# Kernel optimization log

Hardware: AMD Instinct MI355X
Metric: run time of the kernel (lower is better)

## Reference

```python
import jax, jax.numpy as jnp
import numpy as np

N_NODES = 100000
N_EDGES = 1600000
IN_CH, HID_CH, OUT_CH = 128, 256, 128


def _sage_conv(x, src, dst, W_l, b_l, W_r, n_nodes):
    """PyG SAGEConv with mean aggregation: lin_l(mean_j x_j) + lin_r(x)."""
    # gather source features per edge, scatter-sum into destination nodes
    agg = jax.ops.segment_sum(x[src], dst, num_segments=n_nodes)  # [N, C]
    deg = jax.ops.segment_sum(jnp.ones((src.shape[0],), x.dtype), dst,
                              num_segments=n_nodes)               # [N]
    mean = agg / jnp.maximum(deg, 1.0)[:, None]
    return mean @ W_l + b_l + x @ W_r


def setup_inputs() -> dict:
    key = jax.random.key(0)
    ks = jax.random.split(key, 8)
    x = jax.random.normal(ks[0], (N_NODES, IN_CH), dtype=jnp.float32)
    edge_index = jax.random.randint(ks[1], (2, N_EDGES), 0, N_NODES, dtype=jnp.int64)
    s1 = 1.0 / np.sqrt(IN_CH)
    s2 = 1.0 / np.sqrt(HID_CH)
    W1_l = jax.random.normal(ks[2], (IN_CH, HID_CH), dtype=jnp.float32) * s1
    W1_r = jax.random.normal(ks[3], (IN_CH, HID_CH), dtype=jnp.float32) * s1
    b1 = jnp.zeros((HID_CH,), dtype=jnp.float32)
    W2_l = jax.random.normal(ks[4], (HID_CH, OUT_CH), dtype=jnp.float32) * s2
    W2_r = jax.random.normal(ks[5], (HID_CH, OUT_CH), dtype=jnp.float32) * s2
    b2 = jnp.zeros((OUT_CH,), dtype=jnp.float32)
    return {"x": x, "edge_index": edge_index, "W1_l": W1_l, "b1": b1,
            "W1_r": W1_r, "W2_l": W2_l, "b2": b2, "W2_r": W2_r}


def reference(x, edge_index, W1_l, b1, W1_r, W2_l, b2, W2_r):
    src, dst = edge_index[0], edge_index[1]
    h = _sage_conv(x, src, dst, W1_l, b1, W1_r, N_NODES)
    h = jax.nn.relu(h)
    out = _sage_conv(h, src, dst, W2_l, b2, W2_r, N_NODES)
    return out
```

## Files before the change

kernel.cpp:

```cpp
#include <hip/hip_runtime.h>
#include <cstddef>

#define N_NODES_C 100000
#define N_EDGES_C 1600000

#define NPB 64
#define NB 1563
#define SENT_ROW 100000

#define NCB 392
#define CAP 5120
#define SC_EPB 4096
#define SC_BLOCKS 391

#define CONV1_BLOCKS 1563
#define CONV2_BLOCKS 1562

typedef unsigned short u16;
typedef __attribute__((ext_vector_type(8))) short bf16x8;
typedef __attribute__((ext_vector_type(4))) float f32x4;

__device__ __forceinline__ u16 f2bf(float f) {
    unsigned u = __float_as_uint(f);
    u += 0x7fffu + ((u >> 16) & 1);
    return (u16)(u >> 16);
}
__device__ __forceinline__ float lo16f(unsigned v) {
    return __uint_as_float(v << 16);
}
__device__ __forceinline__ float hi16f(unsigned v) {
    return __uint_as_float(v & 0xffff0000u);
}

__device__ __forceinline__ void conv_chunk(const float* __restrict__ x,
                                           u16* __restrict__ x_bf, int i) {
    float4 v = ((const float4*)x)[i];
    ushort4 o;
    o.x = f2bf(v.x); o.y = f2bf(v.y); o.z = f2bf(v.z); o.w = f2bf(v.w);
    ((ushort4*)x_bf)[i] = o;
}


__global__ __launch_bounds__(1024) void prep_a(
    const float* __restrict__ W1l, const float* __restrict__ W1r,
    const float* __restrict__ W2l, const float* __restrict__ W2r,
    u16* __restrict__ T1l, u16* __restrict__ T1r,
    u16* __restrict__ T2l, u16* __restrict__ T2r,
    int* __restrict__ ccursor, u16* __restrict__ x_bf, u16* __restrict__ p2z) {
    const int b = blockIdx.x;
    const int t = threadIdx.x;
    if (b < 128) {
        int id = b * 1024 + t;
        int which = id >> 15;
        int r = id & 32767;
        if (which == 0) {
            int n = r >> 7, k = r & 127;
            T1l[r] = f2bf(W1l[k * 256 + n]);
        } else if (which == 1) {
            int n = r >> 7, k = r & 127;
            T1r[r] = f2bf(W1r[k * 256 + n]);
        } else if (which == 2) {
            int n = r >> 8, k = r & 255;
            T2l[r] = f2bf(W2l[k * 128 + n]);
        } else {
            int n = r >> 8, k = r & 255;
            T2r[r] = f2bf(W2r[k * 128 + n]);
        }
    } else {
        if (t < NCB) ccursor[t] = 0;
        uint4 z; z.x = 0; z.y = 0; z.z = 0; z.w = 0;
        if (t >= 512 && t < 528)
            ((uint4*)(x_bf + (size_t)SENT_ROW * 128))[t - 512] = z;
        else if (t >= 528 && t < 544)
            ((uint4*)(p2z + (size_t)SENT_ROW * 128))[t - 528] = z;
    }
}


__global__ __launch_bounds__(1024) void scatter_conv(
    const int* __restrict__ src, const int* __restrict__ dst,
    int* __restrict__ ccursor, unsigned* __restrict__ epkt2,
    const float* __restrict__ x, u16* __restrict__ x_bf) {
    __shared__ unsigned spkt[SC_EPB];
    __shared__ unsigned short scb[SC_EPB];
    __shared__ int hist[NCB], lstart[NCB], lcur[NCB], grun[NCB], stmp[NCB];

    const int t = threadIdx.x;
    const int b = blockIdx.x;
    if (b >= SC_BLOCKS) {
        conv_chunk(x, x_bf, (b - SC_BLOCKS) * 1024 + t);
        return;
    }
    const int e0 = b * SC_EPB;
    const int cnt = min(SC_EPB, N_EDGES_C - e0);

    if (t < NCB) hist[t] = 0;
    __syncthreads();

    int4 dd, ss;
    int i4 = (e0 >> 2) + t;
    int vi = (i4 * 4 < N_EDGES_C);
    if (vi) {
        dd = ((const int4*)dst)[i4];
        ss = ((const int4*)src)[i4];
        atomicAdd(&hist[dd.x >> 8], 1);
        atomicAdd(&hist[dd.y >> 8], 1);
        atomicAdd(&hist[dd.z >> 8], 1);
        atomicAdd(&hist[dd.w >> 8], 1);
    }
    __syncthreads();

    if (t < NCB) stmp[t] = hist[t];
    __syncthreads();
    for (int off = 1; off < NCB; off <<= 1) {
        int v = 0;
        if (t < NCB && t >= off) v = stmp[t - off];
        __syncthreads();
        if (t < NCB) stmp[t] += v;
        __syncthreads();
    }
    if (t < NCB) {
        int excl = stmp[t] - hist[t];
        lstart[t] = excl;
        lcur[t] = excl;
        if (hist[t])
            grun[t] = t * CAP + atomicAdd(&ccursor[t], hist[t]);
    }
    __syncthreads();

    if (vi) {
        {
            int cb = dd.x >> 8;
            int pos = atomicAdd(&lcur[cb], 1);
            spkt[pos] = ((unsigned)(dd.x & 255) << 17) | (unsigned)ss.x;
            scb[pos] = (unsigned short)cb;
        }
        {
            int cb = dd.y >> 8;
            int pos = atomicAdd(&lcur[cb], 1);
            spkt[pos] = ((unsigned)(dd.y & 255) << 17) | (unsigned)ss.y;
            scb[pos] = (unsigned short)cb;
        }
        {
            int cb = dd.z >> 8;
            int pos = atomicAdd(&lcur[cb], 1);
            spkt[pos] = ((unsigned)(dd.z & 255) << 17) | (unsigned)ss.z;
            scb[pos] = (unsigned short)cb;
        }
        {
            int cb = dd.w >> 8;
            int pos = atomicAdd(&lcur[cb], 1);
            spkt[pos] = ((unsigned)(dd.w & 255) << 17) | (unsigned)ss.w;
            scb[pos] = (unsigned short)cb;
        }
    }
    __syncthreads();

#pragma unroll
    for (int k = 0; k < SC_EPB / 1024; ++k) {
        int i = k * 1024 + t;
        if (i < cnt) {
            int cb = scb[i];
            epkt2[grun[cb] + (i - lstart[cb])] = spkt[i];
        }
    }
}


__global__ __launch_bounds__(1024) void sort_conv(
    const int* __restrict__ ccursor, const unsigned* __restrict__ epkt2,
    unsigned* __restrict__ esrc, int* __restrict__ deg, int* __restrict__ base,
    const float* __restrict__ x, u16* __restrict__ x_bf) {
    __shared__ int hist[256], lstart[256], lcur[256], stmp[256];
    const int t = threadIdx.x;
    const int c = blockIdx.x;
    if (c >= NCB) {
        conv_chunk(x, x_bf, 1600512 + (c - NCB) * 1024 + t);
        return;
    }
    const int s0 = c * CAP;
    int cnt = ccursor[c];
    if (cnt > CAP) cnt = CAP;

    if (t < 256) hist[t] = 0;
    __syncthreads();

    for (int i = t; i < cnt; i += 1024)
        atomicAdd(&hist[epkt2[s0 + i] >> 17], 1);
    __syncthreads();

    if (t < 256) stmp[t] = hist[t];
    __syncthreads();
    for (int off = 1; off < 256; off <<= 1) {
        int v = 0;
        if (t < 256 && t >= off) v = stmp[t - off];
        __syncthreads();
        if (t < 256) stmp[t] += v;
        __syncthreads();
    }
    if (t < 256) {
        int excl = stmp[t] - hist[t];
        lstart[t] = excl;
        lcur[t] = excl;
        int node = c * 256 + t;
        if (node < N_NODES_C) {
            deg[node] = hist[t];
            base[node] = s0 + excl;
        }
    }
    __syncthreads();

    for (int i = t; i < cnt; i += 1024) {
        unsigned p = epkt2[s0 + i];
        int pos = atomicAdd(&lcur[p >> 17], 1);
        esrc[s0 + pos] = p & 0x1ffffu;
    }
}


__global__ __launch_bounds__(512, 8) void fused_gemm_agg(
    const u16* __restrict__ x_bf, const int* __restrict__ deg,
    const int* __restrict__ base, const unsigned* __restrict__ esrc,
    const u16* __restrict__ T1l, const u16* __restrict__ T1r,
    const u16* __restrict__ T2l, const u16* __restrict__ T2r,
    const float* __restrict__ b1, const float* __restrict__ b2,
    u16* __restrict__ p2, u16* __restrict__ outp, int M) {
    alignas(16) __shared__ u16 uni[64 * 256];
    alignas(16) __shared__ u16 Bs[4096];

    u16* const meanS = uni;
    u16* const xS = uni + 64 * 128;
    u16* const hfrag = uni;

    const int tid = threadIdx.x;
    const int lane = tid & 63;
    const int wave = tid >> 6;
    const int qm = lane & 15;
    const int quad = lane >> 4;
    const int b = blockIdx.x;
    const int m0 = b * 64;

#pragma unroll
    for (int r = 0; r < 2; ++r) {
        int c = r * 512 + tid;
        int row = c >> 4, q16 = c & 15;
        __builtin_amdgcn_global_load_lds(
            (const __attribute__((address_space(1))) unsigned*)(
                x_bf + (size_t)(m0 + row) * 128 + ((q16 ^ (row & 7)) * 8)),
            (__attribute__((address_space(3))) unsigned*)(xS + c * 8), 16, 0, 0);
    }

    const int li8 = qm * 8;
    const int gbase = lane & 48;

    for (int pass = 0; pass < 2; ++pass) {
        int n = pass * 32 + wave * 4 + quad;
        int node = m0 + n;
        int d = 0, s0 = 0;
        if (node < N_NODES_C) { d = deg[node]; s0 = base[node]; }
        int dmax = max(d, __shfl_xor(d, 16, 64));
        dmax = max(dmax, __shfl_xor(dmax, 32, 64));

        float a0 = 0.f, a1 = 0.f, a2 = 0.f, a3 = 0.f;
        float a4 = 0.f, a5 = 0.f, a6 = 0.f, a7 = 0.f;

        for (int j = 0; j < dmax; j += 16) {
            int jj = j + qm;
            unsigned sidx = (jj < d) ? esrc[s0 + jj] : (unsigned)SENT_ROW;
            for (int u = 0; u < 16 && j + u < dmax; u += 4) {
                unsigned i0 = __shfl(sidx, gbase + u, 64);
                unsigned i1 = __shfl(sidx, gbase + u + 1, 64);
                unsigned i2 = __shfl(sidx, gbase + u + 2, 64);
                unsigned i3 = __shfl(sidx, gbase + u + 3, 64);
                uint4 r0 = *(const uint4*)(x_bf + (size_t)i0 * 128 + li8);
                uint4 r1 = *(const uint4*)(x_bf + (size_t)i1 * 128 + li8);
                uint4 r2 = *(const uint4*)(x_bf + (size_t)i2 * 128 + li8);
                uint4 r3 = *(const uint4*)(x_bf + (size_t)i3 * 128 + li8);
                a0 += lo16f(r0.x); a1 += hi16f(r0.x);
                a2 += lo16f(r0.y); a3 += hi16f(r0.y);
                a4 += lo16f(r0.z); a5 += hi16f(r0.z);
                a6 += lo16f(r0.w); a7 += hi16f(r0.w);
                a0 += lo16f(r1.x); a1 += hi16f(r1.x);
                a2 += lo16f(r1.y); a3 += hi16f(r1.y);
                a4 += lo16f(r1.z); a5 += hi16f(r1.z);
                a6 += lo16f(r1.w); a7 += hi16f(r1.w);
                a0 += lo16f(r2.x); a1 += hi16f(r2.x);
                a2 += lo16f(r2.y); a3 += hi16f(r2.y);
                a4 += lo16f(r2.z); a5 += hi16f(r2.z);
                a6 += lo16f(r2.w); a7 += hi16f(r2.w);
                a0 += lo16f(r3.x); a1 += hi16f(r3.x);
                a2 += lo16f(r3.y); a3 += hi16f(r3.y);
                a4 += lo16f(r3.z); a5 += hi16f(r3.z);
                a6 += lo16f(r3.w); a7 += hi16f(r3.w);
            }
        }

        float inv = d > 0 ? 1.f / (float)d : 0.f;
        uint4 o;
        o.x = (unsigned)f2bf(a0 * inv) | ((unsigned)f2bf(a1 * inv) << 16);
        o.y = (unsigned)f2bf(a2 * inv) | ((unsigned)f2bf(a3 * inv) << 16);
        o.z = (unsigned)f2bf(a4 * inv) | ((unsigned)f2bf(a5 * inv) << 16);
        o.w = (unsigned)f2bf(a6 * inv) | ((unsigned)f2bf(a7 * inv) << 16);
        *(uint4*)(meanS + n * 128 + ((qm ^ (n & 7)) * 8)) = o;
    }
    __syncthreads();

    const int wr0 = (wave >> 1) * 16;
    const int wcA = (wave & 1) * 64;
    f32x4 acch[8];
#pragma unroll
    for (int j = 0; j < 8; ++j) acch[j] = (f32x4){0.f, 0.f, 0.f, 0.f};

#pragma unroll
    for (int mat = 0; mat < 2; ++mat) {
        const u16* __restrict__ W = mat ? T1r : T1l;
        const u16* Al = mat ? xS : meanS;
#pragma unroll
        for (int k0 = 0; k0 < 128; k0 += 32) {
            int ch0 = k0 >> 3;
            int rowA = wr0 + qm;
            bf16x8 af = *(const bf16x8*)(Al + rowA * 128 +
                                         (((ch0 + quad) ^ (rowA & 7)) * 8));
#pragma unroll
            for (int h = 0; h < 2; ++h) {
                {
                    int c = tid;
                    int row = c >> 2, kc = c & 3;
                    __builtin_amdgcn_global_load_lds(
                        (const __attribute__((address_space(1))) unsigned*)(
                            W + (size_t)(h * 128 + row) * 128 + k0 +
                            ((kc ^ (row & 3)) * 8)),
                        (__attribute__((address_space(3))) unsigned*)(Bs + c * 8),
                        16, 0, 0);
                }
                __syncthreads();
#pragma unroll
                for (int j = 0; j < 4; ++j) {
                    int rB = wcA + j * 16 + qm;
                    bf16x8 bv = *(const bf16x8*)(Bs + rB * 32 +
                                                 ((quad ^ (rB & 3)) * 8));
                    acch[h * 4 + j] = __builtin_amdgcn_mfma_f32_16x16x32_bf16(
                        af, bv, acch[h * 4 + j], 0, 0, 0);
                }
                __syncthreads();
            }
        }
    }

#pragma unroll
    for (int h = 0; h < 2; ++h) {
#pragma unroll
        for (int j = 0; j < 4; ++j) {
            int n = h * 128 + wcA + j * 16 + qm;
            float bb = b1[n];
            int ks = n >> 5, quadB = (n >> 3) & 3, jB = n & 7;
#pragma unroll
            for (int r = 0; r < 4; ++r) {
                int mloc = wr0 + quad * 4 + r;
                float v = fmaxf(acch[h * 4 + j][r] + bb, 0.f);
                hfrag[((ks * 4 + (mloc >> 4)) * 16 + (mloc & 15)) * 32 +
                      quadB * 8 + jB] = f2bf(v);
            }
        }
    }
    __syncthreads();

    const int wrB = (wave >> 1) * 16;
    const int wcB = (wave & 1) * 64;
    f32x4 accp[4], acco[4];
#pragma unroll
    for (int j = 0; j < 4; ++j) {
        accp[j] = (f32x4){0.f, 0.f, 0.f, 0.f};
        acco[j] = (f32x4){0.f, 0.f, 0.f, 0.f};
    }

#pragma unroll
    for (int ks = 0; ks < 8; ++ks) {
        bf16x8 af = *(const bf16x8*)(hfrag +
                                     ((ks * 4 + (wrB >> 4)) * 16 + qm) * 32 + quad * 8);
#pragma unroll
        for (int half = 0; half < 2; ++half) {
            const u16* W = half ? T2r : T2l;
            {
                int c = tid;
                int row = c >> 2, kc = c & 3;
                __builtin_amdgcn_global_load_lds(
                    (const __attribute__((address_space(1))) unsigned*)(
                        W + (size_t)row * 256 + ks * 32 + ((kc ^ (row & 3)) * 8)),
                    (__attribute__((address_space(3))) unsigned*)(Bs + c * 8),
                    16, 0, 0);
            }
            __syncthreads();
            f32x4* acc = half ? acco : accp;
#pragma unroll
            for (int j = 0; j < 4; ++j) {
                int rB = wcB + j * 16 + qm;
                bf16x8 bv = *(const bf16x8*)(Bs + rB * 32 +
                                             ((quad ^ (rB & 3)) * 8));
                acc[j] = __builtin_amdgcn_mfma_f32_16x16x32_bf16(af, bv,
                                                                 acc[j], 0, 0, 0);
            }
            __syncthreads();
        }
    }

#pragma unroll
    for (int j = 0; j < 4; ++j) {
        int n = wcB + j * 16 + qm;
        float bb2 = b2[n];
#pragma unroll
        for (int r = 0; r < 4; ++r) {
            int row = m0 + wrB + quad * 4 + r;
            if (row < M) {
                p2[(size_t)row * 128 + n] = f2bf(accp[j][r]);
                outp[(size_t)row * 128 + n] = f2bf(acco[j][r] + bb2);
            }
        }
    }
}


__global__ __launch_bounds__(256, 8) void agg_final(const u16* __restrict__ tbl,
                                                    const int* __restrict__ deg,
                                                    const int* __restrict__ base,
                                                    const unsigned* __restrict__ esrc,
                                                    const u16* __restrict__ resid,
                                                    float* __restrict__ outv) {
    const int t = threadIdx.x;
    const int wave = t >> 6;
    const int lane = t & 63;
    const int qm = lane & 15;
    const int quad = lane >> 4;
    const int b = blockIdx.x;
    const int li8 = qm * 8;
    const int gbase = lane & 48;

    for (int pass = 0; pass < 4; ++pass) {
        int n = pass * 16 + wave * 4 + quad;
        int node = b * NPB + n;
        bool valid = node < N_NODES_C;
        int d = 0, s0 = 0;
        if (valid) { d = deg[node]; s0 = base[node]; }
        int dmax = max(d, __shfl_xor(d, 16, 64));
        dmax = max(dmax, __shfl_xor(dmax, 32, 64));

        float a0 = 0.f, a1 = 0.f, a2 = 0.f, a3 = 0.f;
        float a4 = 0.f, a5 = 0.f, a6 = 0.f, a7 = 0.f;

        for (int j = 0; j < dmax; j += 16) {
            int jj = j + qm;
            unsigned sidx = (jj < d) ? esrc[s0 + jj] : (unsigned)SENT_ROW;
            for (int u = 0; u < 16 && j + u < dmax; u += 4) {
                unsigned i0 = __shfl(sidx, gbase + u, 64);
                unsigned i1 = __shfl(sidx, gbase + u + 1, 64);
                unsigned i2 = __shfl(sidx, gbase + u + 2, 64);
                unsigned i3 = __shfl(sidx, gbase + u + 3, 64);
                uint4 r0 = *(const uint4*)(tbl + (size_t)i0 * 128 + li8);
                uint4 r1 = *(const uint4*)(tbl + (size_t)i1 * 128 + li8);
                uint4 r2 = *(const uint4*)(tbl + (size_t)i2 * 128 + li8);
                uint4 r3 = *(const uint4*)(tbl + (size_t)i3 * 128 + li8);
                a0 += lo16f(r0.x); a1 += hi16f(r0.x);
                a2 += lo16f(r0.y); a3 += hi16f(r0.y);
                a4 += lo16f(r0.z); a5 += hi16f(r0.z);
                a6 += lo16f(r0.w); a7 += hi16f(r0.w);
                a0 += lo16f(r1.x); a1 += hi16f(r1.x);
                a2 += lo16f(r1.y); a3 += hi16f(r1.y);
                a4 += lo16f(r1.z); a5 += hi16f(r1.z);
                a6 += lo16f(r1.w); a7 += hi16f(r1.w);
                a0 += lo16f(r2.x); a1 += hi16f(r2.x);
                a2 += lo16f(r2.y); a3 += hi16f(r2.y);
                a4 += lo16f(r2.z); a5 += hi16f(r2.z);
                a6 += lo16f(r2.w); a7 += hi16f(r2.w);
                a0 += lo16f(r3.x); a1 += hi16f(r3.x);
                a2 += lo16f(r3.y); a3 += hi16f(r3.y);
                a4 += lo16f(r3.z); a5 += hi16f(r3.z);
                a6 += lo16f(r3.w); a7 += hi16f(r3.w);
            }
        }

        if (valid) {
            float inv = d > 0 ? 1.f / (float)d : 0.f;
            uint4 rp = *(const uint4*)(resid + (size_t)node * 128 + li8);
            float* op = outv + (size_t)node * 128 + li8;
            float4 o0, o1;
            o0.x = a0 * inv + lo16f(rp.x);
            o0.y = a1 * inv + hi16f(rp.x);
            o0.z = a2 * inv + lo16f(rp.y);
            o0.w = a3 * inv + hi16f(rp.y);
            o1.x = a4 * inv + lo16f(rp.z);
            o1.y = a5 * inv + hi16f(rp.z);
            o1.z = a6 * inv + lo16f(rp.w);
            o1.w = a7 * inv + hi16f(rp.w);
            *(float4*)op = o0;
            *(float4*)(op + 4) = o1;
        }
    }
}


extern "C" void kernel_launch(void* const* d_in, const int* in_sizes, int n_in,
                              void* d_out, int out_size, void* d_ws, size_t ws_size,
                              hipStream_t stream) {
    const float* x = (const float*)d_in[0];
    const int* ei = (const int*)d_in[1];
    const float* W1l = (const float*)d_in[2];
    const float* b1 = (const float*)d_in[3];
    const float* W1r = (const float*)d_in[4];
    const float* W2l = (const float*)d_in[5];
    const float* b2 = (const float*)d_in[6];
    const float* W2r = (const float*)d_in[7];
    float* out = (float*)d_out;

    const int* src = ei;
    const int* dst = ei + N_EDGES_C;

    int* iw = (int*)d_ws;
    int* ccursor = iw;
    int* deg = iw + 512;
    int* base = iw + 100864;
    unsigned* epkt2 = (unsigned*)(iw + 201216);
    unsigned* esrc = (unsigned*)(iw + 2208256);
    u16* T1l = (u16*)(iw + 4215296);
    u16* T1r = T1l + 32768;
    u16* T2l = T1r + 32768;
    u16* T2r = T2l + 32768;
    u16* ub = (u16*)((char*)d_ws + (20u << 20));
    u16* x_bf = ub;
    u16* p2 = ub + 12850000;
    u16* outp = ub + 25700000;

    prep_a<<<129, 1024, 0, stream>>>(W1l, W1r, W2l, W2r, T1l, T1r, T2l, T2r,
                                     ccursor, x_bf, p2);
    scatter_conv<<<SC_BLOCKS + CONV1_BLOCKS, 1024, 0, stream>>>(
        src, dst, ccursor, epkt2, x, x_bf);
    sort_conv<<<NCB + CONV2_BLOCKS, 1024, 0, stream>>>(
        ccursor, epkt2, esrc, deg, base, x, x_bf);

    fused_gemm_agg<<<NB, 512, 0, stream>>>(x_bf, deg, base, esrc, T1l, T1r, T2l,
                                           T2r, b1, b2, p2, outp, N_NODES_C);
    agg_final<<<NB, 256, 0, stream>>>(p2, deg, base, esrc, outp, out);
}
```

Baseline: 331.0 us.

## Merge weight prep into scatter kernel and double edges per scatter block

Removes the separate prep_a launch: the weight transpose and bf16 conversion and the sentinel-row zeroing now run as extra blocks inside scatter_conv, and ccursor is cleared with hipMemsetAsync. Each scatter block now handles 8192 edges (two int4 loads per thread), which halves the scatter block count and the per-block histogram and scan overhead. The goal is fewer kernel launches and less fixed cost per block. It adds a memset node, doubles shared memory use per scatter block, and may lower occupancy.

```diff
diff --git a/kernel.cpp b/kernel.cpp
--- a/kernel.cpp
+++ b/kernel.cpp
@@ -10,9 +10,10 @@
 
 #define NCB 392
 #define CAP 5120
-#define SC_EPB 4096
-#define SC_BLOCKS 391
-
+#define SC_EPB 8192
+#define SC_BLOCKS 196
+
+#define WB_BLOCKS 128
 #define CONV1_BLOCKS 1563
 #define CONV2_BLOCKS 1562
 
@@ -41,46 +42,14 @@
 }
 
 
-__global__ __launch_bounds__(1024) void prep_a(
+__global__ __launch_bounds__(1024) void scatter_conv(
+    const int* __restrict__ src, const int* __restrict__ dst,
+    int* __restrict__ ccursor, unsigned* __restrict__ epkt2,
     const float* __restrict__ W1l, const float* __restrict__ W1r,
     const float* __restrict__ W2l, const float* __restrict__ W2r,
     u16* __restrict__ T1l, u16* __restrict__ T1r,
     u16* __restrict__ T2l, u16* __restrict__ T2r,
-    int* __restrict__ ccursor, u16* __restrict__ x_bf, u16* __restrict__ p2z) {
-    const int b = blockIdx.x;
-    const int t = threadIdx.x;
-    if (b < 128) {
-        int id = b * 1024 + t;
-        int which = id >> 15;
-        int r = id & 32767;
-        if (which == 0) {
-            int n = r >> 7, k = r & 127;
-            T1l[r] = f2bf(W1l[k * 256 + n]);
-        } else if (which == 1) {
-            int n = r >> 7, k = r & 127;
-            T1r[r] = f2bf(W1r[k * 256 + n]);
-        } else if (which == 2) {
-            int n = r >> 8, k = r & 255;
-            T2l[r] = f2bf(W2l[k * 128 + n]);
-        } else {
-            int n = r >> 8, k = r & 255;
-            T2r[r] = f2bf(W2r[k * 128 + n]);
-        }
-    } else {
-        if (t < NCB) ccursor[t] = 0;
-        uint4 z; z.x = 0; z.y = 0; z.z = 0; z.w = 0;
-        if (t >= 512 && t < 528)
-            ((uint4*)(x_bf + (size_t)SENT_ROW * 128))[t - 512] = z;
-        else if (t >= 528 && t < 544)
-            ((uint4*)(p2z + (size_t)SENT_ROW * 128))[t - 528] = z;
-    }
-}
-
-
-__global__ __launch_bounds__(1024) void scatter_conv(
-    const int* __restrict__ src, const int* __restrict__ dst,
-    int* __restrict__ ccursor, unsigned* __restrict__ epkt2,
-    const float* __restrict__ x, u16* __restrict__ x_bf) {
+    const float* __restrict__ x, u16* __restrict__ x_bf, u16* __restrict__ p2z) {
     __shared__ unsigned spkt[SC_EPB];
     __shared__ unsigned short scb[SC_EPB];
     __shared__ int hist[NCB], lstart[NCB], lcur[NCB], grun[NCB], stmp[NCB];
@@ -88,7 +57,32 @@
     const int t = threadIdx.x;
     const int b = blockIdx.x;
     if (b >= SC_BLOCKS) {
-        conv_chunk(x, x_bf, (b - SC_BLOCKS) * 1024 + t);
+        if (b < SC_BLOCKS + WB_BLOCKS) {
+            int id = (b - SC_BLOCKS) * 1024 + t;
+            int which = id >> 15;
+            int r = id & 32767;
+            if (which == 0) {
+                int n = r >> 7, k = r & 127;
+                T1l[r] = f2bf(W1l[k * 256 + n]);
+            } else if (which == 1) {
+                int n = r >> 7, k = r & 127;
+                T1r[r] = f2bf(W1r[k * 256 + n]);
+            } else if (which == 2) {
+                int n = r >> 8, k = r & 255;
+                T2l[r] = f2bf(W2l[k * 128 + n]);
+            } else {
+                int n = r >> 8, k = r & 255;
+                T2r[r] = f2bf(W2r[k * 128 + n]);
+            }
+        } else if (b == SC_BLOCKS + WB_BLOCKS) {
+            uint4 z; z.x = 0; z.y = 0; z.z = 0; z.w = 0;
+            if (t < 16)
+                ((uint4*)(x_bf + (size_t)SENT_ROW * 128))[t] = z;
+            else if (t < 32)
+                ((uint4*)(p2z + (size_t)SENT_ROW * 128))[t - 16] = z;
+        } else {
+            conv_chunk(x, x_bf, (b - SC_BLOCKS - WB_BLOCKS - 1) * 1024 + t);
+        }
         return;
     }
     const int e0 = b * SC_EPB;
@@ -97,16 +91,20 @@
     if (t < NCB) hist[t] = 0;
     __syncthreads();
 
-    int4 dd, ss;
-    int i4 = (e0 >> 2) + t;
-    int vi = (i4 * 4 < N_EDGES_C);
-    if (vi) {
-        dd = ((const int4*)dst)[i4];
-        ss = ((const int4*)src)[i4];
-        atomicAdd(&hist[dd.x >> 8], 1);
-        atomicAdd(&hist[dd.y >> 8], 1);
-        atomicAdd(&hist[dd.z >> 8], 1);
-        atomicAdd(&hist[dd.w >> 8], 1);
+    int4 dd[2], ss[2];
+    int vi[2];
+#pragma unroll
+    for (int r = 0; r < 2; ++r) {
+        int i = (e0 >> 2) + r * 1024 + t;
+        vi[r] = (i * 4 < N_EDGES_C);
+        if (vi[r]) {
+            dd[r] = ((const int4*)dst)[i];
+            ss[r] = ((const int4*)src)[i];
+            atomicAdd(&hist[dd[r].x >> 8], 1);
+            atomicAdd(&hist[dd[r].y >> 8], 1);
+            atomicAdd(&hist[dd[r].z >> 8], 1);
+            atomicAdd(&hist[dd[r].w >> 8], 1);
+        }
     }
     __syncthreads();
 
@@ -128,30 +126,35 @@
     }
     __syncthreads();
 
-    if (vi) {
-        {
-            int cb = dd.x >> 8;
-            int pos = atomicAdd(&lcur[cb], 1);
-            spkt[pos] = ((unsigned)(dd.x & 255) << 17) | (unsigned)ss.x;
-            scb[pos] = (unsigned short)cb;
-        }
-        {
-            int cb = dd.y >> 8;
-            int pos = atomicAdd(&lcur[cb], 1);
-            spkt[pos] = ((unsigned)(dd.y & 255) << 17) | (unsigned)ss.y;
-            scb[pos] = (unsigned short)cb;
-        }
-        {
-            int cb = dd.z >> 8;
-            int pos = atomicAdd(&lcur[cb], 1);
-            spkt[pos] = ((unsigned)(dd.z & 255) << 17) | (unsigned)ss.z;
-            scb[pos] = (unsigned short)cb;
-        }
-        {
-            int cb = dd.w >> 8;
-            int pos = atomicAdd(&lcur[cb], 1);
-            spkt[pos] = ((unsigned)(dd.w & 255) << 17) | (unsigned)ss.w;
-            scb[pos] = (unsigned short)cb;
+#pragma unroll
+    for (int r = 0; r < 2; ++r) {
+        if (vi[r]) {
+            int4 d = dd[r];
+            int4 s4 = ss[r];
+            {
+                int cb = d.x >> 8;
+                int pos = atomicAdd(&lcur[cb], 1);
+                spkt[pos] = ((unsigned)(d.x & 255) << 17) | (unsigned)s4.x;
+                scb[pos] = (unsigned short)cb;
+            }
+            {
+                int cb = d.y >> 8;
+                int pos = atomicAdd(&lcur[cb], 1);
+                spkt[pos] = ((unsigned)(d.y & 255) << 17) | (unsigned)s4.y;
+                scb[pos] = (unsigned short)cb;
+            }
+            {
+                int cb = d.z >> 8;
+                int pos = atomicAdd(&lcur[cb], 1);
+                spkt[pos] = ((unsigned)(d.z & 255) << 17) | (unsigned)s4.z;
+                scb[pos] = (unsigned short)cb;
+            }
+            {
+                int cb = d.w >> 8;
+                int pos = atomicAdd(&lcur[cb], 1);
+                spkt[pos] = ((unsigned)(d.w & 255) << 17) | (unsigned)s4.w;
+                scb[pos] = (unsigned short)cb;
+            }
         }
     }
     __syncthreads();
@@ -529,10 +532,11 @@
     u16* p2 = ub + 12850000;
     u16* outp = ub + 25700000;
 
-    prep_a<<<129, 1024, 0, stream>>>(W1l, W1r, W2l, W2r, T1l, T1r, T2l, T2r,
-                                     ccursor, x_bf, p2);
-    scatter_conv<<<SC_BLOCKS + CONV1_BLOCKS, 1024, 0, stream>>>(
-        src, dst, ccursor, epkt2, x, x_bf);
+    hipMemsetAsync(ccursor, 0, NCB * sizeof(int), stream);
+
+    scatter_conv<<<SC_BLOCKS + WB_BLOCKS + 1 + CONV1_BLOCKS, 1024, 0, stream>>>(
+        src, dst, ccursor, epkt2, W1l, W1r, W2l, W2r, T1l, T1r, T2l, T2r,
+        x, x_bf, p2);
     sort_conv<<<NCB + CONV2_BLOCKS, 1024, 0, stream>>>(
         ccursor, epkt2, esrc, deg, base, x, x_bf);
 
```

Result: no change. 325.8 us (-1.6%).
